# Kernel tuning notes

Hardware: AMD Instinct MI355X
Metric: run time of the kernel (lower is better)

The kernel has to match this reference:

```python
import jax, jax.numpy as jnp
import numpy as np

H, W = 800, 800          # map height/width (Encoder init args)
B, N, SD = 1, 100000, 32 # batch, entity_num, scatter_dim
C = 8                    # number of spatial grids
SPATIAL = (120, 120)     # SPATIAL_SIZE


def setup_inputs() -> dict:
    key = jax.random.key(0)
    ks = jax.random.split(key, 8)
    return {
        "spatial": jax.random.normal(ks[0], (C, H, W), jnp.float32) * 200.0,
        "project_embeddings": jax.random.normal(ks[1], (B, N, SD), jnp.float32),
        "locations": jax.random.randint(ks[2], (B, N, 2), 0, 800, jnp.int64 if jax.config.jax_enable_x64 else jnp.int32),
        "scalar": jax.random.normal(ks[3], (B, 8), jnp.float32),
        "w1": jax.random.normal(ks[4], (8, 32), jnp.float32) * 0.35,
        "b1": jnp.zeros((32,), jnp.float32),
        "w2": jax.random.normal(ks[5], (32, 4), jnp.float32) * 0.25,
        "b2": jnp.zeros((4,), jnp.float32),
    }


def _scatter_connection(project_embeddings, locations):
    # project_embeddings: [B, N, SD], locations: [B, N, 2] (x, y) ints
    loc = locations.reshape(-1, 2)
    x = jnp.clip(loc[:, 0], 0, W - 1)
    y = jnp.clip(loc[:, 1], 0, H - 1)
    bias = jnp.repeat(jnp.arange(B, dtype=x.dtype), N) * (H * W)
    idx = y * W + x + bias                       # [B*N] flat indices into B*H*W
    src = project_embeddings.reshape(-1, SD).T   # [SD, B*N]
    smap = jnp.zeros((SD, B * H * W), project_embeddings.dtype)
    smap = smap.at[:, idx].add(src)              # duplicate-safe scatter_add
    smap = smap.reshape(SD, B, H, W).transpose(1, 0, 2, 3)  # [B, SD, H, W]
    return jax.image.resize(smap, (B, SD) + SPATIAL, method="bilinear")


def _process_grids(spatial):
    # crop is the full map (grid of ones -> all rows/cols kept)
    arr = jnp.nan_to_num(spatial, posinf=0.0)
    arr = jnp.where(arr > 255.0, 255.0, arr) / 255.0
    arr = jnp.rot90(arr, k=1, axes=(1, 2))       # torch rot90 default: CCW in last-2 dims
    arr = jax.image.resize(arr, (C,) + SPATIAL, method="bilinear")
    return arr.astype(jnp.float32)[None]         # [1, C, 120, 120]


def reference(spatial, project_embeddings, locations, scalar, w1, b1, w2, b2):
    scatter_entity = _scatter_connection(project_embeddings, locations)  # [B,32,120,120]
    processed_spatial = _process_grids(spatial)                          # [1, C,120,120]
    final_spatial = jnp.concatenate([processed_spatial, scatter_entity], axis=1)
    scalar_embeddings = jax.nn.relu(scalar @ w1 + b1)
    scalar_embeddings = jax.nn.relu(scalar_embeddings @ w2 + b2)
    return final_spatial, scalar_embeddings
```

## Files before the change

kernel.cpp:

```cpp
#include <hip/hip_runtime.h>
#include <hip/hip_bf16.h>
#include <math.h>

#define HMAP 800
#define WMAP 800
#define OHW  120
#define NCELL (OHW * OHW)
#define NCH  8
#define NPTS 100000
#define SDIM 32
#define CAP  32
#define NBIN1 121
#define NBINS (NBIN1 * NBIN1)

__device__ __forceinline__ float rscale() { return 800.0f / 120.0f; }

__device__ __forceinline__ float clipval(float v) {
    if (isnan(v)) v = 0.f;
    else if (isinf(v)) v = (v > 0.f) ? 0.f : -3.4028234663852886e38f;
    if (v > 255.f) v = 255.f;
    return v;
}

__device__ __forceinline__ float norm_sum(int i) {
    const float r = rscale();
    float c = ((float)i + 0.5f) * r - 0.5f;
    int j0 = (int)ceilf(c - r);
    float s = 0.f;
#pragma unroll
    for (int k = 0; k < 14; ++k) {
        int j = j0 + k;
        if (j < 0 || j >= HMAP) continue;
        s += fmaxf(0.f, 1.f - fabsf(c - (float)j) / r);
    }
    return s;
}

#define WS_COUNTS   0
#define WS_SPILLCUR 14641
#define WS_INVS     14656
#define WS_ENTRIES  14784
#define WS_SPILL    (WS_ENTRIES + NBINS * CAP * 2)
#define WS_T        (WS_SPILL + NPTS * 2)
#define WS_END      (WS_T + NCH * WMAP * OHW)
#define WS_REQ_BYTES ((size_t)WS_END * 4)

#define ZERO_BLOCKS 58
#define FILL_BLOCKS ((NPTS + 127) / 128)
#define RY_BLOCKS   (NCH * WMAP)
#define GA_BLOCKS   (NCELL / 4)
#define RX_BLOCKS   (NCH * OHW / 2)

__global__ void k_zero(int* __restrict__ counts, float* __restrict__ invS) {
    int gid = blockIdx.x * 256 + threadIdx.x;
    if (gid < 14656) counts[gid] = 0;
    if (gid < OHW) invS[gid] = 1.0f / norm_sum(gid);
}

__global__ void k_phase1(const float* __restrict__ spatial, const int* __restrict__ loc,
                         float* __restrict__ T, int* __restrict__ counts,
                         int2* __restrict__ entries, int2* __restrict__ spill,
                         int* __restrict__ spill_cur, const float* __restrict__ invS) {
    __shared__ float row[HMAP];
    if (blockIdx.x < FILL_BLOCKS) {
        int n = blockIdx.x * 128 + threadIdx.x;
        if (n >= NPTS) return;
        int2 xy = ((const int2*)loc)[n];
        int x = min(max(xy.x, 0), WMAP - 1);
        int y = min(max(xy.y, 0), HMAP - 1);
        const float r = rscale();
        int iy0 = (int)floorf(((float)y + 0.5f) / r - 0.5f);
        int ix0 = (int)floorf(((float)x + 0.5f) / r - 0.5f);
        int bin = (iy0 + 1) * NBIN1 + (ix0 + 1);
        int pos = (y << 10) | x;
        int slot = atomicAdd(&counts[bin], 1);
        if (slot < CAP) {
            entries[(size_t)bin * CAP + slot] = make_int2(n, pos);
        } else {
            int s = atomicAdd(spill_cur, 1);
            if (s < NPTS) spill[s] = make_int2((bin << 17) | n, pos);
        }
        return;
    }
    int bx = blockIdx.x - FILL_BLOCKS;
    int c = bx / WMAP, xx = bx % WMAP;
    const float* rp = spatial + (size_t)c * (HMAP * WMAP) + (size_t)xx * WMAP;
    for (int j = threadIdx.x; j < HMAP; j += 128) row[j] = clipval(rp[j]);
    __syncthreads();
    int oy = threadIdx.x;
    if (oy >= OHW) return;
    const float r = rscale();
    const float invR = 1.0f / r;
    float cy = ((float)oy + 0.5f) * r - 0.5f;
    int y0 = (int)ceilf(cy - r);
    float acc = 0.f;
#pragma unroll
    for (int k = 0; k < 14; ++k) {
        int j = y0 + k;
        float w = fmaxf(0.f, fmaf(-fabsf(cy - (float)j), invR, 1.f));
        w = (j >= 0 && j < HMAP) ? w : 0.f;
        int jc = min(max(j, 0), HMAP - 1);
        acc = fmaf(w, row[HMAP - 1 - jc], acc);
    }
    T[((size_t)c * WMAP + xx) * OHW + oy] = acc * (1.0f / 255.0f) * invS[oy];
}

__global__ void k_phase2(const float* __restrict__ T, const float* __restrict__ emb,
                         const int* __restrict__ counts, const int2* __restrict__ entries,
                         const int2* __restrict__ spill, const int* __restrict__ spill_cur,
                         const float* __restrict__ invS, float* __restrict__ out,
                         const float* __restrict__ scalar, const float* __restrict__ w1,
                         const float* __restrict__ b1, const float* __restrict__ w2,
                         const float* __restrict__ b2) {
    __shared__ int2 st[4][4][CAP];
    __shared__ float sh[32];
    int bid = blockIdx.x;
    if (bid < GA_BLOCKS) {
        int sbid = (bid & 7) * (GA_BLOCKS / 8) + (bid >> 3);
        int t = threadIdx.x;
        int wv = t >> 6;
        int cell = sbid * 4 + wv;
        int lane = t & 63;
        int g = lane >> 4;
        int c2 = lane & 15;
        int iy = cell / OHW, ix = cell % OHW;
        const float r = rscale();
        const float invR = 1.0f / r;
        float cy = ((float)iy + 0.5f) * r - 0.5f;
        float cx = ((float)ix + 0.5f) * r - 0.5f;
        float invS2 = invS[iy] * invS[ix];
        int b00 = iy * NBIN1 + ix;

        int mybin = b00 + (g >> 1) * NBIN1 + (g & 1);
        int craw = counts[mybin];
        bool ovfany = __any(craw > CAP);
        int cnt = min(craw, CAP);
        int cmax = cnt;
        cmax = max(cmax, __shfl_xor(cmax, 16));
        cmax = max(cmax, __shfl_xor(cmax, 32));

#pragma unroll
        for (int ch = 0; ch < 2; ++ch) {
            int binrow = b00 + ch * NBIN1;
            const int2* base = entries + (size_t)binrow * CAP;
            int2 e = base[lane];
            int gs = ch * 2 + (lane >> 5);
            int slot = lane & 31;
            int scnt = min(counts[binrow + (lane >> 5)], CAP);
            int idx = 0;
            float w = 0.f;
            if (slot < scnt) {
                float py = (float)((e.y >> 10) & 1023);
                float px = (float)(e.y & 1023);
                float wy = fmaxf(0.f, fmaf(-fabsf(cy - py), invR, 1.f));
                float wx = fmaxf(0.f, fmaf(-fabsf(cx - px), invR, 1.f));
                w = wy * wx * invS2;
                idx = e.x;
            }
            st[wv][gs][slot] = make_int2(idx, __float_as_int(w));
        }

        const float2* embp = (const float2*)emb;
        float ax = 0.f, ay = 0.f;
        for (int i = 0; i < cmax; i += 4) {
            int2 s0 = st[wv][g][i + 0];
            int2 s1 = st[wv][g][i + 1];
            int2 s2 = st[wv][g][i + 2];
            int2 s3 = st[wv][g][i + 3];
            float2 v0 = embp[(size_t)s0.x * (SDIM / 2) + c2];
            float2 v1 = embp[(size_t)s1.x * (SDIM / 2) + c2];
            float2 v2 = embp[(size_t)s2.x * (SDIM / 2) + c2];
            float2 v3 = embp[(size_t)s3.x * (SDIM / 2) + c2];
            float w0 = __int_as_float(s0.y), w1_ = __int_as_float(s1.y);
            float w2_ = __int_as_float(s2.y), w3 = __int_as_float(s3.y);
            ax = fmaf(w0, v0.x, ax); ay = fmaf(w0, v0.y, ay);
            ax = fmaf(w1_, v1.x, ax); ay = fmaf(w1_, v1.y, ay);
            ax = fmaf(w2_, v2.x, ax); ay = fmaf(w2_, v2.y, ay);
            ax = fmaf(w3, v3.x, ax); ay = fmaf(w3, v3.y, ay);
        }

        if (ovfany) {
            int sn = min(spill_cur[0], NPTS);
            for (int s = 0; s < sn; ++s) {
                int2 e = spill[s];
                if ((e.x >> 17) == mybin) {
                    int n = e.x & 0x1FFFF;
                    float py = (float)((e.y >> 10) & 1023);
                    float px = (float)(e.y & 1023);
                    float wy = fmaxf(0.f, fmaf(-fabsf(cy - py), invR, 1.f));
                    float wx = fmaxf(0.f, fmaf(-fabsf(cx - px), invR, 1.f));
                    float w = wy * wx * invS2;
                    float2 v = embp[(size_t)n * (SDIM / 2) + c2];
                    ax = fmaf(w, v.x, ax); ay = fmaf(w, v.y, ay);
                }
            }
        }

        ax += __shfl_xor(ax, 16); ay += __shfl_xor(ay, 16);
        ax += __shfl_xor(ax, 32); ay += __shfl_xor(ay, 32);
        if (lane < 16) {
            out[(size_t)(NCH + 2 * c2) * NCELL + cell] = ax;
            out[(size_t)(NCH + 2 * c2 + 1) * NCELL + cell] = ay;
        }
        return;
    }
    if (bid < GA_BLOCKS + RX_BLOCKS) {
        int col = (bid - GA_BLOCKS) * 2 + (threadIdx.x >> 7);
        int oy = threadIdx.x & 127;
        if (oy >= OHW) return;
        int c = col / OHW, ox = col % OHW;
        const float r = rscale();
        const float invR = 1.0f / r;
        float cx = ((float)ox + 0.5f) * r - 0.5f;
        int x0 = (int)ceilf(cx - r);
        float acc = 0.f;
#pragma unroll
        for (int k = 0; k < 14; ++k) {
            int j = x0 + k;
            float w = fmaxf(0.f, fmaf(-fabsf(cx - (float)j), invR, 1.f));
            w = (j >= 0 && j < WMAP) ? w : 0.f;
            int jc = min(max(j, 0), WMAP - 1);
            acc = fmaf(w, T[((size_t)c * WMAP + jc) * OHW + oy], acc);
        }
        out[((size_t)c * OHW + oy) * OHW + ox] = acc * invS[ox];
        return;
    }
    int j = threadIdx.x;
    if (j < 32) {
        float a = b1[j];
        for (int i = 0; i < 8; ++i) a = fmaf(scalar[i], w1[i * 32 + j], a);
        sh[j] = fmaxf(a, 0.f);
    }
    __syncthreads();
    if (j < 4) {
        float a = b2[j];
        for (int i = 0; i < 32; ++i) a = fmaf(sh[i], w2[i * 4 + j], a);
        out[(size_t)(NCH + SDIM) * NCELL + j] = fmaxf(a, 0.f);
    }
}

__global__ void k_norm_fb(float* __restrict__ S) {
    int i = blockIdx.x * blockDim.x + threadIdx.x;
    if (i < OHW) S[i] = norm_sum(i);
}

__global__ void k_spatial_fb(const float* __restrict__ spatial, const float* __restrict__ S,
                             float* __restrict__ out) {
    int t = blockIdx.x * blockDim.x + threadIdx.x;
    if (t >= NCH * NCELL) return;
    int c = t / NCELL, rem = t % NCELL;
    int oy = rem / OHW, ox = rem % OHW;
    const float r = rscale();
    float cy = ((float)oy + 0.5f) * r - 0.5f;
    float cx = ((float)ox + 0.5f) * r - 0.5f;
    int y0 = (int)ceilf(cy - r);
    int x0 = (int)ceilf(cx - r);
    const float* sp = spatial + (size_t)c * (HMAP * WMAP);
    float acc = 0.f;
    for (int kx = 0; kx < 14; ++kx) {
        int col = x0 + kx;
        if (col < 0 || col >= WMAP) continue;
        float wxx = fmaxf(0.f, 1.f - fabsf(cx - (float)col) / r);
        if (wxx == 0.f) continue;
        const float* colp = sp + (size_t)col * WMAP;
        float accy = 0.f;
        for (int ky = 0; ky < 14; ++ky) {
            int j = y0 + ky;
            if (j < 0 || j >= HMAP) continue;
            float wyy = fmaxf(0.f, 1.f - fabsf(cy - (float)j) / r);
            accy = fmaf(wyy, clipval(colp[HMAP - 1 - j]), accy);
        }
        acc = fmaf(wxx, accy, acc);
    }
    out[t] = acc * (1.0f / 255.0f) / (S[oy] * S[ox]);
}

__global__ void k_scatter_fb(const float* __restrict__ emb, const int* __restrict__ loc,
                             const float* __restrict__ S, float* __restrict__ out) {
    int t = blockIdx.x * blockDim.x + threadIdx.x;
    if (t >= NPTS * SDIM) return;
    int n = t >> 5, c = t & 31;
    int x = min(max(loc[2 * n + 0], 0), WMAP - 1);
    int y = min(max(loc[2 * n + 1], 0), HMAP - 1);
    float e = emb[t];
    const float r = rscale();
    int iy0 = (int)floorf(((float)y + 0.5f) / r - 0.5f);
    int ix0 = (int)floorf(((float)x + 0.5f) / r - 0.5f);
    float* base = out + (size_t)(NCH + c) * NCELL;
#pragma unroll
    for (int a = 0; a < 2; ++a) {
        int iy = iy0 + a;
        if (iy < 0 || iy >= OHW) continue;
        float cyv = ((float)iy + 0.5f) * r - 0.5f;
        float wy = fmaxf(0.f, 1.f - fabsf(cyv - (float)y) / r) / S[iy];
#pragma unroll
        for (int b = 0; b < 2; ++b) {
            int ix = ix0 + b;
            if (ix < 0 || ix >= OHW) continue;
            float cxv = ((float)ix + 0.5f) * r - 0.5f;
            float wx = fmaxf(0.f, 1.f - fabsf(cxv - (float)x) / r) / S[ix];
            atomicAdd(base + iy * OHW + ix, e * wy * wx);
        }
    }
}

__global__ void k_mlp_fb(const float* __restrict__ scalar, const float* __restrict__ w1,
                         const float* __restrict__ b1, const float* __restrict__ w2,
                         const float* __restrict__ b2, float* __restrict__ out) {
    __shared__ float h[32];
    int j = threadIdx.x;
    if (j < 32) {
        float a = b1[j];
        for (int i = 0; i < 8; ++i) a = fmaf(scalar[i], w1[i * 32 + j], a);
        h[j] = fmaxf(a, 0.f);
    }
    __syncthreads();
    if (j < 4) {
        float a = b2[j];
        for (int i = 0; i < 32; ++i) a = fmaf(h[i], w2[i * 4 + j], a);
        out[(size_t)(NCH + SDIM) * NCELL + j] = fmaxf(a, 0.f);
    }
}

extern "C" void kernel_launch(void* const* d_in, const int* in_sizes, int n_in,
                              void* d_out, int out_size, void* d_ws, size_t ws_size,
                              hipStream_t stream) {
    const float* spatial = (const float*)d_in[0];
    const float* emb     = (const float*)d_in[1];
    const int*   loc     = (const int*)d_in[2];
    const float* scalar  = (const float*)d_in[3];
    const float* w1      = (const float*)d_in[4];
    const float* b1      = (const float*)d_in[5];
    const float* w2      = (const float*)d_in[6];
    const float* b2      = (const float*)d_in[7];
    float* out = (float*)d_out;

    int*   wsi = (int*)d_ws;
    float* wsf = (float*)d_ws;

    if (ws_size >= WS_REQ_BYTES) {
        int*   counts    = wsi + WS_COUNTS;
        int*   spill_cur = wsi + WS_SPILLCUR;
        float* invS      = wsf + WS_INVS;
        int2*  entries   = (int2*)(wsi + WS_ENTRIES);
        int2*  spill     = (int2*)(wsi + WS_SPILL);
        float* T         = wsf + WS_T;

        k_zero<<<ZERO_BLOCKS, 256, 0, stream>>>(counts, invS);
        k_phase1<<<FILL_BLOCKS + RY_BLOCKS, 128, 0, stream>>>(spatial, loc, T, counts,
                                                              entries, spill, spill_cur,
                                                              invS);
        k_phase2<<<GA_BLOCKS + RX_BLOCKS + 1, 256, 0, stream>>>(T, emb, counts, entries,
                                                                spill, spill_cur, invS,
                                                                out, scalar, w1, b1,
                                                                w2, b2);
    } else {
        float* S = wsf;
        hipMemsetAsync(d_out, 0, (size_t)out_size * sizeof(float), stream);
        k_norm_fb<<<1, 128, 0, stream>>>(S);
        k_spatial_fb<<<(NCH * NCELL + 255) / 256, 256, 0, stream>>>(spatial, S, out);
        k_scatter_fb<<<(NPTS * SDIM + 255) / 256, 256, 0, stream>>>(emb, loc, S, out);
        k_mlp_fb<<<1, 64, 0, stream>>>(scalar, w1, b1, w2, b2, out);
    }
}
```

Measured before the change: 36.15 us.

## Regroup kernels: merge zeroing with row resample, split entity binning out

Moves the vertical resample of the spatial grids into the zeroing kernel. It now runs one thread per output element, reads global memory directly instead of staging rows in shared memory, and computes the normalisation weight inline. Entity binning moves into its own kernel launched afterwards. The aim is to remove the shared-memory staging and the block-level sync, and to cut idle threads in the 128-thread blocks. In exchange it adds a kernel launch and does redundant clipped global loads across threads.

```diff
diff --git a/kernel.cpp b/kernel.cpp
--- a/kernel.cpp
+++ b/kernel.cpp
@@ -45,64 +45,61 @@
 #define WS_END      (WS_T + NCH * WMAP * OHW)
 #define WS_REQ_BYTES ((size_t)WS_END * 4)
 
-#define ZERO_BLOCKS 58
-#define FILL_BLOCKS ((NPTS + 127) / 128)
-#define RY_BLOCKS   (NCH * WMAP)
+#define Z_BLOCKS    58
+#define RY_BLOCKS   (NCH * WMAP * OHW / 256)
+#define FILL_BLOCKS ((NPTS + 255) / 256)
 #define GA_BLOCKS   (NCELL / 4)
 #define RX_BLOCKS   (NCH * OHW / 2)
 
-__global__ void k_zero(int* __restrict__ counts, float* __restrict__ invS) {
-    int gid = blockIdx.x * 256 + threadIdx.x;
-    if (gid < 14656) counts[gid] = 0;
-    if (gid < OHW) invS[gid] = 1.0f / norm_sum(gid);
-}
-
-__global__ void k_phase1(const float* __restrict__ spatial, const int* __restrict__ loc,
-                         float* __restrict__ T, int* __restrict__ counts,
-                         int2* __restrict__ entries, int2* __restrict__ spill,
-                         int* __restrict__ spill_cur, const float* __restrict__ invS) {
-    __shared__ float row[HMAP];
-    if (blockIdx.x < FILL_BLOCKS) {
-        int n = blockIdx.x * 128 + threadIdx.x;
-        if (n >= NPTS) return;
-        int2 xy = ((const int2*)loc)[n];
-        int x = min(max(xy.x, 0), WMAP - 1);
-        int y = min(max(xy.y, 0), HMAP - 1);
-        const float r = rscale();
-        int iy0 = (int)floorf(((float)y + 0.5f) / r - 0.5f);
-        int ix0 = (int)floorf(((float)x + 0.5f) / r - 0.5f);
-        int bin = (iy0 + 1) * NBIN1 + (ix0 + 1);
-        int pos = (y << 10) | x;
-        int slot = atomicAdd(&counts[bin], 1);
-        if (slot < CAP) {
-            entries[(size_t)bin * CAP + slot] = make_int2(n, pos);
-        } else {
-            int s = atomicAdd(spill_cur, 1);
-            if (s < NPTS) spill[s] = make_int2((bin << 17) | n, pos);
-        }
+__global__ void k_zerory(const float* __restrict__ spatial, int* __restrict__ counts,
+                         float* __restrict__ invS, float* __restrict__ T) {
+    if (blockIdx.x < Z_BLOCKS) {
+        int gid = blockIdx.x * 256 + threadIdx.x;
+        if (gid < 14656) counts[gid] = 0;
+        if (gid < OHW) invS[gid] = 1.0f / norm_sum(gid);
         return;
     }
-    int bx = blockIdx.x - FILL_BLOCKS;
-    int c = bx / WMAP, xx = bx % WMAP;
-    const float* rp = spatial + (size_t)c * (HMAP * WMAP) + (size_t)xx * WMAP;
-    for (int j = threadIdx.x; j < HMAP; j += 128) row[j] = clipval(rp[j]);
-    __syncthreads();
-    int oy = threadIdx.x;
-    if (oy >= OHW) return;
+    int t = (blockIdx.x - Z_BLOCKS) * 256 + threadIdx.x;
+    int oy  = t % OHW;
+    int cxx = t / OHW;
+    const float* rp = spatial + (size_t)cxx * WMAP;
     const float r = rscale();
     const float invR = 1.0f / r;
     float cy = ((float)oy + 0.5f) * r - 0.5f;
     int y0 = (int)ceilf(cy - r);
-    float acc = 0.f;
+    float acc = 0.f, ws = 0.f;
 #pragma unroll
     for (int k = 0; k < 14; ++k) {
         int j = y0 + k;
         float w = fmaxf(0.f, fmaf(-fabsf(cy - (float)j), invR, 1.f));
         w = (j >= 0 && j < HMAP) ? w : 0.f;
         int jc = min(max(j, 0), HMAP - 1);
-        acc = fmaf(w, row[HMAP - 1 - jc], acc);
-    }
-    T[((size_t)c * WMAP + xx) * OHW + oy] = acc * (1.0f / 255.0f) * invS[oy];
+        ws += w;
+        acc = fmaf(w, clipval(rp[HMAP - 1 - jc]), acc);
+    }
+    T[t] = acc / (255.f * ws);
+}
+
+__global__ void k_fill(const int* __restrict__ loc, int* __restrict__ counts,
+                       int2* __restrict__ entries, int2* __restrict__ spill,
+                       int* __restrict__ spill_cur) {
+    int n = blockIdx.x * 256 + threadIdx.x;
+    if (n >= NPTS) return;
+    int2 xy = ((const int2*)loc)[n];
+    int x = min(max(xy.x, 0), WMAP - 1);
+    int y = min(max(xy.y, 0), HMAP - 1);
+    const float r = rscale();
+    int iy0 = (int)floorf(((float)y + 0.5f) / r - 0.5f);
+    int ix0 = (int)floorf(((float)x + 0.5f) / r - 0.5f);
+    int bin = (iy0 + 1) * NBIN1 + (ix0 + 1);
+    int pos = (y << 10) | x;
+    int slot = atomicAdd(&counts[bin], 1);
+    if (slot < CAP) {
+        entries[(size_t)bin * CAP + slot] = make_int2(n, pos);
+    } else {
+        int s = atomicAdd(spill_cur, 1);
+        if (s < NPTS) spill[s] = make_int2((bin << 17) | n, pos);
+    }
 }
 
 __global__ void k_phase2(const float* __restrict__ T, const float* __restrict__ emb,
@@ -346,10 +343,8 @@
         int2*  spill     = (int2*)(wsi + WS_SPILL);
         float* T         = wsf + WS_T;
 
-        k_zero<<<ZERO_BLOCKS, 256, 0, stream>>>(counts, invS);
-        k_phase1<<<FILL_BLOCKS + RY_BLOCKS, 128, 0, stream>>>(spatial, loc, T, counts,
-                                                              entries, spill, spill_cur,
-                                                              invS);
+        k_zerory<<<Z_BLOCKS + RY_BLOCKS, 256, 0, stream>>>(spatial, counts, invS, T);
+        k_fill<<<FILL_BLOCKS, 256, 0, stream>>>(loc, counts, entries, spill, spill_cur);
         k_phase2<<<GA_BLOCKS + RX_BLOCKS + 1, 256, 0, stream>>>(T, emb, counts, entries,
                                                                 spill, spill_cur, invS,
                                                                 out, scalar, w1, b1,
```

New measurement: 39.56 us. 1.09x slower.
